# Kernel tuning notes

Measured on AMD Instinct MI355X. Metric: run time of the kernel, lower is better.

The kernel has to match this reference:

```python
import jax, jax.numpy as jnp
import numpy as np

N = 50000        # nodes
E = 800000       # edges (before self-loops)
F_IN = 128       # input features
HID = 32         # per-head hidden channels
H1 = 4           # heads of conv1
H2 = 8           # heads of conv2
NEG_SLOPE = 0.2  # PyG GATConv LeakyReLU slope
E_DEC = 100000   # pos/neg decode edges each


def setup_inputs() -> dict:
    key = jax.random.key(0)
    ks = jax.random.split(key, 12)
    s = 0.1
    return {
        "x": jax.random.normal(ks[0], (N, F_IN), jnp.float32),
        "edge_index": jax.random.randint(ks[1], (2, E), 0, N, dtype=jnp.int32),
        "pos_edge_index": jax.random.randint(ks[2], (2, E_DEC), 0, N, dtype=jnp.int32),
        "neg_edge_index": jax.random.randint(ks[3], (2, E_DEC), 0, N, dtype=jnp.int32),
        "W1": jax.random.normal(ks[4], (F_IN, H1 * HID), jnp.float32) * s,
        "a_src1": jax.random.normal(ks[5], (H1, HID), jnp.float32) * s,
        "a_dst1": jax.random.normal(ks[6], (H1, HID), jnp.float32) * s,
        "b1": jax.random.normal(ks[7], (H1 * HID,), jnp.float32) * s,
        "W2": jax.random.normal(ks[8], (H1 * HID, H2 * HID), jnp.float32) * s,
        "a_src2": jax.random.normal(ks[9], (H2, HID), jnp.float32) * s,
        "a_dst2": jax.random.normal(ks[10], (H2, HID), jnp.float32) * s,
        "b2": jax.random.normal(ks[11], (H2 * HID,), jnp.float32) * s,
    }


def _segment_softmax(e, seg, n):
    # softmax over edges grouped by destination node; max is detached (cancels analytically)
    m = jax.lax.stop_gradient(jax.ops.segment_max(e, seg, num_segments=n))
    ex = jnp.exp(e - m[seg])
    denom = jax.ops.segment_sum(ex, seg, num_segments=n)
    return ex / (denom[seg] + 1e-16)


def _gat_conv(x, src, dst, W, a_src, a_dst, b, heads, out_ch):
    n = x.shape[0]
    h = (x @ W).reshape(n, heads, out_ch)             # [N,H,C]
    al_s = (h * a_src[None]).sum(-1)                  # [N,H]
    al_d = (h * a_dst[None]).sum(-1)                  # [N,H]
    e = al_s[src] + al_d[dst]                         # [E,H] edge logits
    e = jnp.where(e > 0, e, NEG_SLOPE * e)            # LeakyReLU
    alpha = _segment_softmax(e, dst, n)               # [E,H]
    msg = h[src] * alpha[:, :, None]                  # [E,H,C]
    out = jax.ops.segment_sum(msg, dst, num_segments=n)  # [N,H,C]
    return out.reshape(n, heads * out_ch) + b


def reference(x, edge_index, pos_edge_index, neg_edge_index,
              W1, a_src1, a_dst1, b1, W2, a_src2, a_dst2, b2):
    n = x.shape[0]
    loops = jnp.arange(n, dtype=edge_index.dtype)     # PyG add_self_loops=True
    src = jnp.concatenate([edge_index[0], loops])
    dst = jnp.concatenate([edge_index[1], loops])
    # encode
    z = jax.nn.relu(_gat_conv(x, src, dst, W1, a_src1, a_dst1, b1, H1, HID))
    z = _gat_conv(z, src, dst, W2, a_src2, a_dst2, b2, H2, HID)
    # decode
    ei = jnp.concatenate([pos_edge_index, neg_edge_index], axis=1)
    logits = (z[ei[0]] * z[ei[1]]).sum(-1)            # [2*E_DEC]
    return logits
```

## Files before the change

kernel.cpp:

```cpp
#include <hip/hip_runtime.h>
#include <hip/hip_bf16.h>

#define NN 50000
#define EE 800000
#define ET (EE + NN)
#define F_IN 128
#define HID 32
#define H1 4
#define H2 8
#define E_DEC 100000
#define NEG_SLOPE 0.2f

typedef __attribute__((ext_vector_type(8))) short short8;
typedef __attribute__((ext_vector_type(4))) float floatx4;

__device__ __forceinline__ unsigned short f2b(float f) {
    __hip_bfloat16 h = __float2bfloat16(f);
    return *reinterpret_cast<unsigned short*>(&h);
}
__device__ __forceinline__ float b2f(unsigned short u) {
    return __uint_as_float(((unsigned int)u) << 16);
}

__device__ __forceinline__ void packW_one(const float* __restrict__ W,
                                          unsigned short* __restrict__ Wp, int OUT, int id) {
    const int ctg = id >> 8;
    const int ln = id & 63;
    const int col = ctg * 16 + (ln & 15);
    const int k0 = ((id >> 6) & 3) * 32 + ((ln >> 4) & 3) * 8;
    ushort4 lo, hi;
    lo.x = f2b(W[(k0 + 0) * OUT + col]);
    lo.y = f2b(W[(k0 + 1) * OUT + col]);
    lo.z = f2b(W[(k0 + 2) * OUT + col]);
    lo.w = f2b(W[(k0 + 3) * OUT + col]);
    hi.x = f2b(W[(k0 + 4) * OUT + col]);
    hi.y = f2b(W[(k0 + 5) * OUT + col]);
    hi.z = f2b(W[(k0 + 6) * OUT + col]);
    hi.w = f2b(W[(k0 + 7) * OUT + col]);
    ((ushort4*)Wp)[id * 2] = lo;
    ((ushort4*)Wp)[id * 2 + 1] = hi;
}

#define HIST_BLOCKS ((EE / 4 + 255) / 256)
#define PACK_BLOCKS ((6144 + 255) / 256)

__global__ void hist_pack_k(const int* __restrict__ ei, int* __restrict__ counts_p,
                            const int* __restrict__ probe, int* __restrict__ rank,
                            const float* __restrict__ W1, unsigned short* __restrict__ wp1,
                            const float* __restrict__ W2, unsigned short* __restrict__ wp2) {
    if (blockIdx.x < HIST_BLOCKS) {
        const int t = blockIdx.x * 256 + threadIdx.x;
        if (t >= EE / 4) return;
        const int pv = probe[0];
        int* cp = counts_p + (blockIdx.x & 7) * NN;
        const int4 d4 = ((const int4*)(ei + EE))[t];
        int4 r4;
        r4.x = atomicAdd(&cp[d4.x], 1) - pv;
        r4.y = atomicAdd(&cp[d4.y], 1) - pv;
        r4.z = atomicAdd(&cp[d4.z], 1) - pv;
        r4.w = atomicAdd(&cp[d4.w], 1) - pv;
        ((int4*)rank)[t] = r4;
    } else {
        const int id = (blockIdx.x - HIST_BLOCKS) * 256 + threadIdx.x;
        if (id < 2048) packW_one(W1, wp1, 128, id);
        else if (id < 6144) packW_one(W2, wp2, 256, id - 2048);
    }
}

__global__ void scan1_k(const int* __restrict__ counts_p, const int* __restrict__ probe,
                        int* __restrict__ bsum) {
    __shared__ int sh[256];
    const unsigned pv = (unsigned)probe[0];
    int t = threadIdx.x;
    int i = blockIdx.x * 256 + t;
    int deg = 0;
    if (i < NN) {
        unsigned sum = 0;
#pragma unroll
        for (int s = 0; s < 8; ++s) sum += (unsigned)counts_p[s * NN + i];
        deg = (int)(sum - 8u * pv) + 1;
    }
    sh[t] = deg;
    __syncthreads();
    for (int off = 128; off > 0; off >>= 1) {
        if (t < off) sh[t] += sh[t + off];
        __syncthreads();
    }
    if (t == 0) bsum[blockIdx.x] = sh[0];
}

__global__ void scan2_k(int* __restrict__ bsum, int nb, int* __restrict__ start) {
    __shared__ int sh[256];
    int t = threadIdx.x;
    int v = (t < nb) ? bsum[t] : 0;
    sh[t] = v;
    __syncthreads();
    for (int off = 1; off < 256; off <<= 1) {
        int u = (t >= off) ? sh[t - off] : 0;
        __syncthreads();
        sh[t] += u;
        __syncthreads();
    }
    if (t < nb) bsum[t] = sh[t] - v;
    if (t == 0) start[NN] = ET;
}

__global__ void scan3_k(const int* __restrict__ counts_p, const int* __restrict__ probe,
                        const int* __restrict__ bsum, int* __restrict__ start,
                        int* __restrict__ offs, int* __restrict__ csr) {
    __shared__ int sh[256];
    const unsigned pv = (unsigned)probe[0];
    int t = threadIdx.x;
    int i = blockIdx.x * 256 + t;
    int part[8];
    int deg = 0;
    if (i < NN) {
        deg = 1;
#pragma unroll
        for (int s = 0; s < 8; ++s) {
            part[s] = (int)((unsigned)counts_p[s * NN + i] - pv);
            deg += part[s];
        }
    }
    sh[t] = deg;
    __syncthreads();
    for (int off = 1; off < 256; off <<= 1) {
        int u = (t >= off) ? sh[t - off] : 0;
        __syncthreads();
        sh[t] += u;
        __syncthreads();
    }
    int excl = sh[t] - deg + bsum[blockIdx.x];
    if (i < NN) {
        start[i] = excl;
        int o = excl;
#pragma unroll
        for (int s = 0; s < 8; ++s) {
            offs[s * NN + i] = o;
            o += part[s];
        }
        csr[o] = i;
    }
}

__global__ void scatter_k(const int* __restrict__ ei, const int* __restrict__ rank,
                          const int* __restrict__ offs, int* __restrict__ csr) {
    const int t = blockIdx.x * 256 + threadIdx.x;
    if (t >= EE / 4) return;
    const int* off = offs + (blockIdx.x & 7) * NN;
    const int4 s4 = ((const int4*)ei)[t];
    const int4 d4 = ((const int4*)(ei + EE))[t];
    const int4 r4 = ((const int4*)rank)[t];
    csr[off[d4.x] + r4.x] = s4.x;
    csr[off[d4.y] + r4.y] = s4.y;
    csr[off[d4.z] + r4.z] = s4.z;
    csr[off[d4.w] + r4.w] = s4.w;
}

template <int OUT, int H, int CT, bool F32IN>
__global__ void gemm_k(const void* __restrict__ Xin, const unsigned short* __restrict__ Wp,
                       const float* __restrict__ a_src, const float* __restrict__ a_dst,
                       unsigned short* __restrict__ Hout, float* __restrict__ als,
                       float* __restrict__ ald) {
    const int wave = threadIdx.x >> 6;
    const int lane = threadIdx.x & 63;
    const int quad = lane >> 4;
    const int rl = lane & 15;
    const int r0 = blockIdx.x * 64;
    floatx4 acc[4][CT];
#pragma unroll
    for (int rt = 0; rt < 4; ++rt)
#pragma unroll
        for (int ct = 0; ct < CT; ++ct) acc[rt][ct] = {0.f, 0.f, 0.f, 0.f};

#pragma unroll
    for (int ks = 0; ks < 4; ++ks) {
        short8 a[4];
        const int c0k = ks * 32 + quad * 8;
#pragma unroll
        for (int rt = 0; rt < 4; ++rt) {
            int row = r0 + rt * 16 + rl;
            row = row < NN ? row : NN - 1;
            if (F32IN) {
                const float4* xp =
                    (const float4*)((const float*)Xin + (long long)row * 128 + c0k);
                const float4 v0 = xp[0];
                const float4 v1 = xp[1];
                short8 tt;
                tt[0] = (short)f2b(v0.x);
                tt[1] = (short)f2b(v0.y);
                tt[2] = (short)f2b(v0.z);
                tt[3] = (short)f2b(v0.w);
                tt[4] = (short)f2b(v1.x);
                tt[5] = (short)f2b(v1.y);
                tt[6] = (short)f2b(v1.z);
                tt[7] = (short)f2b(v1.w);
                a[rt] = tt;
            } else {
                a[rt] = *(const short8*)((const unsigned short*)Xin +
                                         (long long)row * 128 + c0k);
            }
        }
#pragma unroll
        for (int ct = 0; ct < CT; ++ct) {
            const int ctg = wave * CT + ct;
            const short8 b = *(const short8*)(Wp + (((ctg * 4 + ks) * 64 + lane) << 3));
#pragma unroll
            for (int rt = 0; rt < 4; ++rt)
                acc[rt][ct] = __builtin_amdgcn_mfma_f32_16x16x32_bf16(a[rt], b, acc[rt][ct], 0, 0, 0);
        }
    }
#pragma unroll
    for (int rt = 0; rt < 4; ++rt) {
        const int rowbase = r0 + rt * 16 + quad * 4;
#pragma unroll
        for (int ct = 0; ct < CT; ++ct) {
            const int col = (wave * CT + ct) * 16 + rl;
#pragma unroll
            for (int r = 0; r < 4; ++r) {
                const int row = rowbase + r;
                if (row < NN) Hout[(long long)row * OUT + col] = f2b(acc[rt][ct][r]);
            }
        }
    }
    float asv[CT], adv[CT];
#pragma unroll
    for (int ct = 0; ct < CT; ++ct) {
        const int col = (wave * CT + ct) * 16 + rl;
        asv[ct] = a_src[col];
        adv[ct] = a_dst[col];
    }
#pragma unroll
    for (int rt = 0; rt < 4; ++rt) {
#pragma unroll
        for (int r = 0; r < 4; ++r) {
            const int row = r0 + rt * 16 + quad * 4 + r;
            float ps[CT / 2], pd[CT / 2];
#pragma unroll
            for (int hh = 0; hh < CT / 2; ++hh) {
                ps[hh] = acc[rt][2 * hh][r] * asv[2 * hh] + acc[rt][2 * hh + 1][r] * asv[2 * hh + 1];
                pd[hh] = acc[rt][2 * hh][r] * adv[2 * hh] + acc[rt][2 * hh + 1][r] * adv[2 * hh + 1];
#pragma unroll
                for (int m = 8; m >= 1; m >>= 1) {
                    ps[hh] += __shfl_xor(ps[hh], m, 64);
                    pd[hh] += __shfl_xor(pd[hh], m, 64);
                }
            }
            if (rl == 0 && row < NN) {
#pragma unroll
                for (int hh = 0; hh < CT / 2; ++hh) {
                    const int hd = wave * (CT / 2) + hh;
                    als[(long long)row * H + hd] = ps[hh];
                    ald[(long long)row * H + hd] = pd[hh];
                }
            }
        }
    }
}

__global__ void gather1_k(const int* __restrict__ start, const int* __restrict__ csr,
                          const float* __restrict__ als, const float* __restrict__ ald,
                          const unsigned short* __restrict__ Hin,
                          const float* __restrict__ bias, unsigned short* __restrict__ outp) {
    const int d = blockIdx.x;
    const int lane = threadIdx.x;
    const int cl = lane & 31;
    const int slot = lane >> 5;
    const int hd = cl >> 3;
    const int beg = start[d], end = start[d + 1];
    const float aldd = ald[(long long)d * H1 + hd];
    float a0 = 0.f, a1 = 0.f, a2 = 0.f, a3 = 0.f, den = 0.f;
    int i = beg + slot;
    for (; i + 7 * 2 < end; i += 8 * 2) {
        int s[8];
        float l[8];
        ushort4 hv[8];
#pragma unroll
        for (int k = 0; k < 8; ++k) s[k] = csr[i + k * 2];
#pragma unroll
        for (int k = 0; k < 8; ++k) l[k] = als[(long long)s[k] * H1 + hd] + aldd;
#pragma unroll
        for (int k = 0; k < 8; ++k) hv[k] = *(const ushort4*)(Hin + (long long)s[k] * 128 + cl * 4);
#pragma unroll
        for (int k = 0; k < 8; ++k) {
            float lg = l[k] > 0.f ? l[k] : NEG_SLOPE * l[k];
            const float w = __expf(lg);
            den += w;
            a0 += w * b2f(hv[k].x);
            a1 += w * b2f(hv[k].y);
            a2 += w * b2f(hv[k].z);
            a3 += w * b2f(hv[k].w);
        }
    }
    for (; i + 3 * 2 < end; i += 4 * 2) {
        int s[4];
        float l[4];
        ushort4 hv[4];
#pragma unroll
        for (int k = 0; k < 4; ++k) s[k] = csr[i + k * 2];
#pragma unroll
        for (int k = 0; k < 4; ++k) l[k] = als[(long long)s[k] * H1 + hd] + aldd;
#pragma unroll
        for (int k = 0; k < 4; ++k) hv[k] = *(const ushort4*)(Hin + (long long)s[k] * 128 + cl * 4);
#pragma unroll
        for (int k = 0; k < 4; ++k) {
            float lg = l[k] > 0.f ? l[k] : NEG_SLOPE * l[k];
            const float w = __expf(lg);
            den += w;
            a0 += w * b2f(hv[k].x);
            a1 += w * b2f(hv[k].y);
            a2 += w * b2f(hv[k].z);
            a3 += w * b2f(hv[k].w);
        }
    }
    for (; i < end; i += 2) {
        const int s = csr[i];
        float lg = als[(long long)s * H1 + hd] + aldd;
        lg = lg > 0.f ? lg : NEG_SLOPE * lg;
        const float w = __expf(lg);
        const ushort4 hv = *(const ushort4*)(Hin + (long long)s * 128 + cl * 4);
        den += w;
        a0 += w * b2f(hv.x);
        a1 += w * b2f(hv.y);
        a2 += w * b2f(hv.z);
        a3 += w * b2f(hv.w);
    }
    a0 += __shfl_xor(a0, 32, 64);
    a1 += __shfl_xor(a1, 32, 64);
    a2 += __shfl_xor(a2, 32, 64);
    a3 += __shfl_xor(a3, 32, 64);
    den += __shfl_xor(den, 32, 64);
    if (lane < 32) {
        const float inv = 1.f / (den + 1e-16f);
        const int c0 = cl * 4;
        float v0 = a0 * inv + bias[c0];
        float v1 = a1 * inv + bias[c0 + 1];
        float v2 = a2 * inv + bias[c0 + 2];
        float v3 = a3 * inv + bias[c0 + 3];
        v0 = v0 > 0.f ? v0 : 0.f;
        v1 = v1 > 0.f ? v1 : 0.f;
        v2 = v2 > 0.f ? v2 : 0.f;
        v3 = v3 > 0.f ? v3 : 0.f;
        ushort4 o;
        o.x = f2b(v0);
        o.y = f2b(v1);
        o.z = f2b(v2);
        o.w = f2b(v3);
        *(ushort4*)(outp + (long long)d * 128 + c0) = o;
    }
}

__global__ void gather2_k(const int* __restrict__ start, const int* __restrict__ csr,
                          const float* __restrict__ als, const float* __restrict__ ald,
                          const unsigned short* __restrict__ Hin,
                          const float* __restrict__ bias, unsigned short* __restrict__ outp) {
    const int d = blockIdx.x;
    const int lane = threadIdx.x;
    const int hd = lane >> 3;
    const int beg = start[d], end = start[d + 1];
    const float aldd = ald[(long long)d * H2 + hd];
    float a0 = 0.f, a1 = 0.f, a2 = 0.f, a3 = 0.f, den = 0.f;
    int i = beg;
    for (; i + 7 < end; i += 8) {
        int s[8];
        float l[8];
        ushort4 hv[8];
#pragma unroll
        for (int k = 0; k < 8; ++k) s[k] = csr[i + k];
#pragma unroll
        for (int k = 0; k < 8; ++k) l[k] = als[(long long)s[k] * H2 + hd] + aldd;
#pragma unroll
        for (int k = 0; k < 8; ++k) hv[k] = *(const ushort4*)(Hin + (long long)s[k] * 256 + lane * 4);
#pragma unroll
        for (int k = 0; k < 8; ++k) {
            float lg = l[k] > 0.f ? l[k] : NEG_SLOPE * l[k];
            const float w = __expf(lg);
            den += w;
            a0 += w * b2f(hv[k].x);
            a1 += w * b2f(hv[k].y);
            a2 += w * b2f(hv[k].z);
            a3 += w * b2f(hv[k].w);
        }
    }
    for (; i + 3 < end; i += 4) {
        int s[4];
        float l[4];
        ushort4 hv[4];
#pragma unroll
        for (int k = 0; k < 4; ++k) s[k] = csr[i + k];
#pragma unroll
        for (int k = 0; k < 4; ++k) l[k] = als[(long long)s[k] * H2 + hd] + aldd;
#pragma unroll
        for (int k = 0; k < 4; ++k) hv[k] = *(const ushort4*)(Hin + (long long)s[k] * 256 + lane * 4);
#pragma unroll
        for (int k = 0; k < 4; ++k) {
            float lg = l[k] > 0.f ? l[k] : NEG_SLOPE * l[k];
            const float w = __expf(lg);
            den += w;
            a0 += w * b2f(hv[k].x);
            a1 += w * b2f(hv[k].y);
            a2 += w * b2f(hv[k].z);
            a3 += w * b2f(hv[k].w);
        }
    }
    for (; i < end; ++i) {
        const int s = csr[i];
        float lg = als[(long long)s * H2 + hd] + aldd;
        lg = lg > 0.f ? lg : NEG_SLOPE * lg;
        const float w = __expf(lg);
        const ushort4 hv = *(const ushort4*)(Hin + (long long)s * 256 + lane * 4);
        den += w;
        a0 += w * b2f(hv.x);
        a1 += w * b2f(hv.y);
        a2 += w * b2f(hv.z);
        a3 += w * b2f(hv.w);
    }
    const float inv = 1.f / (den + 1e-16f);
    const int c0 = lane * 4;
    ushort4 o;
    o.x = f2b(a0 * inv + bias[c0]);
    o.y = f2b(a1 * inv + bias[c0 + 1]);
    o.z = f2b(a2 * inv + bias[c0 + 2]);
    o.w = f2b(a3 * inv + bias[c0 + 3]);
    *(ushort4*)(outp + (long long)d * 256 + c0) = o;
}

__global__ void decode_s_k(const int* __restrict__ pei, const int* __restrict__ nei,
                           const unsigned short* __restrict__ z2, float* __restrict__ part) {
    const int s = blockIdx.x & 7;
    const int g = blockIdx.x >> 3;
    const int wave = threadIdx.x >> 6, lane = threadIdx.x & 63;
    const int slot = lane >> 3, cl = lane & 7;
    const int idx = g * 32 + wave * 8 + slot;
    if (idx >= 2 * E_DEC) return;
    int a, b;
    if (idx < E_DEC) {
        a = pei[idx];
        b = pei[E_DEC + idx];
    } else {
        const int j = idx - E_DEC;
        a = nei[j];
        b = nei[E_DEC + j];
    }
    const ushort4 ua = *(const ushort4*)(z2 + (long long)a * 256 + s * 32 + cl * 4);
    const ushort4 ub = *(const ushort4*)(z2 + (long long)b * 256 + s * 32 + cl * 4);
    float sum = b2f(ua.x) * b2f(ub.x) + b2f(ua.y) * b2f(ub.y) +
                b2f(ua.z) * b2f(ub.z) + b2f(ua.w) * b2f(ub.w);
    sum += __shfl_xor(sum, 4, 64);
    sum += __shfl_xor(sum, 2, 64);
    sum += __shfl_xor(sum, 1, 64);
    if (cl == 0) part[(long long)s * (2 * E_DEC) + idx] = sum;
}

__global__ void reduce_k(const float* __restrict__ part, float* __restrict__ out) {
    const int i = blockIdx.x * 256 + threadIdx.x;
    if (i >= 2 * E_DEC) return;
    float s = 0.f;
#pragma unroll
    for (int k = 0; k < 8; ++k) s += part[(long long)k * (2 * E_DEC) + i];
    out[i] = s;
}

extern "C" void kernel_launch(void* const* d_in, const int* in_sizes, int n_in,
                              void* d_out, int out_size, void* d_ws, size_t ws_size,
                              hipStream_t stream) {
    const float* x = (const float*)d_in[0];
    const int* ei = (const int*)d_in[1];
    const int* pei = (const int*)d_in[2];
    const int* nei = (const int*)d_in[3];
    const float* W1 = (const float*)d_in[4];
    const float* as1 = (const float*)d_in[5];
    const float* ad1 = (const float*)d_in[6];
    const float* b1 = (const float*)d_in[7];
    const float* W2 = (const float*)d_in[8];
    const float* as2 = (const float*)d_in[9];
    const float* ad2 = (const float*)d_in[10];
    const float* b2 = (const float*)d_in[11];
    float* out = (float*)d_out;

    unsigned short* h1 = (unsigned short*)d_ws;
    unsigned short* h2 = h1 + (long long)NN * 128;
    unsigned short* z2 = h2 + (long long)NN * 256;
    unsigned short* z1 = z2 + (long long)NN * 256;
    unsigned short* wp1 = z1 + (long long)NN * 128;
    unsigned short* wp2 = wp1 + 128 * 128;
    float* als1 = (float*)(wp2 + 128 * 256);
    float* ald1 = als1 + NN * H1;
    float* als2 = ald1 + NN * H1;
    float* ald2 = als2 + NN * H2;
    float* part = ald2 + NN * H2;
    int* counts_p = (int*)(part + 8 * 2 * E_DEC);
    int* start = counts_p + 8 * NN;
    int* offs = start + NN + 1;
    int* rank = offs + 8 * NN;
    int* bsum = rank + EE;
    int* csr = bsum + 256;
    int* probe = csr + ET;

    const int NB = (NN + 255) / 256;

    hist_pack_k<<<HIST_BLOCKS + PACK_BLOCKS, 256, 0, stream>>>(
        ei, counts_p, probe, rank, W1, wp1, W2, wp2);
    scan1_k<<<NB, 256, 0, stream>>>(counts_p, probe, bsum);
    scan2_k<<<1, 256, 0, stream>>>(bsum, NB, start);
    scan3_k<<<NB, 256, 0, stream>>>(counts_p, probe, bsum, start, offs, csr);
    scatter_k<<<HIST_BLOCKS, 256, 0, stream>>>(ei, rank, offs, csr);

    gemm_k<128, H1, 2, true><<<(NN + 63) / 64, 256, 0, stream>>>(
        x, wp1, as1, ad1, h1, als1, ald1);
    gather1_k<<<NN, 64, 0, stream>>>(start, csr, als1, ald1, h1, b1, z1);

    gemm_k<256, H2, 4, false><<<(NN + 63) / 64, 256, 0, stream>>>(
        z1, wp2, as2, ad2, h2, als2, ald2);
    gather2_k<<<NN, 64, 0, stream>>>(start, csr, als2, ald2, h2, b2, z2);

    decode_s_k<<<8 * ((2 * E_DEC + 31) / 32), 256, 0, stream>>>(pei, nei, z2, part);
    reduce_k<<<(2 * E_DEC + 255) / 256, 256, 0, stream>>>(part, out);
}
```

Before: 334.5 us.

## Store per-head slabs and map head slices to XCDs in gather kernels

The GEMM now writes the projected features as head-major slabs (one [N,32] slab per head) and the attention logits as [H,N]. A single templated gather kernel replaces the two per-layer gathers. Each wave handles one destination node and one head, and the low bits of the block index pick the head slice, so each XCD's L2 only touches one head's slab. The goal is better L2 locality for random source gathers, at the cost of more blocks, re-reading the CSR once per head, and dropping the unrolled multi-load loops, which lowers memory-level parallelism per lane.

```diff
diff --git a/kernel.cpp b/kernel.cpp
--- a/kernel.cpp
+++ b/kernel.cpp
@@ -216,10 +216,11 @@
 #pragma unroll
         for (int ct = 0; ct < CT; ++ct) {
             const int col = (wave * CT + ct) * 16 + rl;
+            unsigned short* hp = Hout + (long long)(col >> 5) * NN * 32 + (col & 31);
 #pragma unroll
             for (int r = 0; r < 4; ++r) {
                 const int row = rowbase + r;
-                if (row < NN) Hout[(long long)row * OUT + col] = f2b(acc[rt][ct][r]);
+                if (row < NN) hp[(long long)row * 32] = f2b(acc[rt][ct][r]);
             }
         }
     }
@@ -250,179 +251,75 @@
 #pragma unroll
                 for (int hh = 0; hh < CT / 2; ++hh) {
                     const int hd = wave * (CT / 2) + hh;
-                    als[(long long)row * H + hd] = ps[hh];
-                    ald[(long long)row * H + hd] = pd[hh];
+                    als[(long long)hd * NN + row] = ps[hh];
+                    ald[(long long)hd * NN + row] = pd[hh];
                 }
             }
         }
     }
 }
 
-__global__ void gather1_k(const int* __restrict__ start, const int* __restrict__ csr,
+template <int OUT, int NSLICE, bool RELU>
+__global__ void gathers_k(const int* __restrict__ start, const int* __restrict__ csr,
                           const float* __restrict__ als, const float* __restrict__ ald,
                           const unsigned short* __restrict__ Hin,
                           const float* __restrict__ bias, unsigned short* __restrict__ outp) {
-    const int d = blockIdx.x;
-    const int lane = threadIdx.x;
-    const int cl = lane & 31;
-    const int slot = lane >> 5;
-    const int hd = cl >> 3;
+    constexpr int SUB = 8 / NSLICE;
+    const int xcd = blockIdx.x & 7;
+    const int s = xcd / SUB;
+    const int sub = xcd & (SUB - 1);
+    const int wave = threadIdx.x >> 6;
+    const int lane = threadIdx.x & 63;
+    const int cl = lane & 7;
+    const int slot = lane >> 3;
+    const int d = (blockIdx.x >> 3) * (4 * SUB) + sub * 4 + wave;
+    if (d >= NN) return;
+    const float* als_h = als + (long long)s * NN;
+    const float aldd = ald[(long long)s * NN + d];
+    const unsigned short* slab = Hin + (long long)s * NN * 32;
     const int beg = start[d], end = start[d + 1];
-    const float aldd = ald[(long long)d * H1 + hd];
     float a0 = 0.f, a1 = 0.f, a2 = 0.f, a3 = 0.f, den = 0.f;
-    int i = beg + slot;
-    for (; i + 7 * 2 < end; i += 8 * 2) {
-        int s[8];
-        float l[8];
-        ushort4 hv[8];
-#pragma unroll
-        for (int k = 0; k < 8; ++k) s[k] = csr[i + k * 2];
-#pragma unroll
-        for (int k = 0; k < 8; ++k) l[k] = als[(long long)s[k] * H1 + hd] + aldd;
-#pragma unroll
-        for (int k = 0; k < 8; ++k) hv[k] = *(const ushort4*)(Hin + (long long)s[k] * 128 + cl * 4);
-#pragma unroll
-        for (int k = 0; k < 8; ++k) {
-            float lg = l[k] > 0.f ? l[k] : NEG_SLOPE * l[k];
-            const float w = __expf(lg);
-            den += w;
-            a0 += w * b2f(hv[k].x);
-            a1 += w * b2f(hv[k].y);
-            a2 += w * b2f(hv[k].z);
-            a3 += w * b2f(hv[k].w);
-        }
-    }
-    for (; i + 3 * 2 < end; i += 4 * 2) {
-        int s[4];
-        float l[4];
-        ushort4 hv[4];
-#pragma unroll
-        for (int k = 0; k < 4; ++k) s[k] = csr[i + k * 2];
-#pragma unroll
-        for (int k = 0; k < 4; ++k) l[k] = als[(long long)s[k] * H1 + hd] + aldd;
-#pragma unroll
-        for (int k = 0; k < 4; ++k) hv[k] = *(const ushort4*)(Hin + (long long)s[k] * 128 + cl * 4);
-#pragma unroll
-        for (int k = 0; k < 4; ++k) {
-            float lg = l[k] > 0.f ? l[k] : NEG_SLOPE * l[k];
-            const float w = __expf(lg);
-            den += w;
-            a0 += w * b2f(hv[k].x);
-            a1 += w * b2f(hv[k].y);
-            a2 += w * b2f(hv[k].z);
-            a3 += w * b2f(hv[k].w);
-        }
-    }
-    for (; i < end; i += 2) {
-        const int s = csr[i];
-        float lg = als[(long long)s * H1 + hd] + aldd;
+    for (int i = beg + slot; i < end; i += 8) {
+        const int src = __builtin_nontemporal_load(csr + i);
+        float lg = als_h[src] + aldd;
         lg = lg > 0.f ? lg : NEG_SLOPE * lg;
         const float w = __expf(lg);
-        const ushort4 hv = *(const ushort4*)(Hin + (long long)s * 128 + cl * 4);
+        const ushort4 hv = *(const ushort4*)(slab + (long long)src * 32 + cl * 4);
         den += w;
         a0 += w * b2f(hv.x);
         a1 += w * b2f(hv.y);
         a2 += w * b2f(hv.z);
         a3 += w * b2f(hv.w);
     }
-    a0 += __shfl_xor(a0, 32, 64);
-    a1 += __shfl_xor(a1, 32, 64);
-    a2 += __shfl_xor(a2, 32, 64);
-    a3 += __shfl_xor(a3, 32, 64);
-    den += __shfl_xor(den, 32, 64);
-    if (lane < 32) {
+#pragma unroll
+    for (int m = 8; m < 64; m <<= 1) {
+        a0 += __shfl_xor(a0, m, 64);
+        a1 += __shfl_xor(a1, m, 64);
+        a2 += __shfl_xor(a2, m, 64);
+        a3 += __shfl_xor(a3, m, 64);
+        den += __shfl_xor(den, m, 64);
+    }
+    if (lane < 8) {
         const float inv = 1.f / (den + 1e-16f);
-        const int c0 = cl * 4;
+        const int c0 = s * 32 + cl * 4;
         float v0 = a0 * inv + bias[c0];
         float v1 = a1 * inv + bias[c0 + 1];
         float v2 = a2 * inv + bias[c0 + 2];
         float v3 = a3 * inv + bias[c0 + 3];
-        v0 = v0 > 0.f ? v0 : 0.f;
-        v1 = v1 > 0.f ? v1 : 0.f;
-        v2 = v2 > 0.f ? v2 : 0.f;
-        v3 = v3 > 0.f ? v3 : 0.f;
-        ushort4 o;
-        o.x = f2b(v0);
-        o.y = f2b(v1);
-        o.z = f2b(v2);
-        o.w = f2b(v3);
-        *(ushort4*)(outp + (long long)d * 128 + c0) = o;
-    }
-}
-
-__global__ void gather2_k(const int* __restrict__ start, const int* __restrict__ csr,
-                          const float* __restrict__ als, const float* __restrict__ ald,
-                          const unsigned short* __restrict__ Hin,
-                          const float* __restrict__ bias, unsigned short* __restrict__ outp) {
-    const int d = blockIdx.x;
-    const int lane = threadIdx.x;
-    const int hd = lane >> 3;
-    const int beg = start[d], end = start[d + 1];
-    const float aldd = ald[(long long)d * H2 + hd];
-    float a0 = 0.f, a1 = 0.f, a2 = 0.f, a3 = 0.f, den = 0.f;
-    int i = beg;
-    for (; i + 7 < end; i += 8) {
-        int s[8];
-        float l[8];
-        ushort4 hv[8];
-#pragma unroll
-        for (int k = 0; k < 8; ++k) s[k] = csr[i + k];
-#pragma unroll
-        for (int k = 0; k < 8; ++k) l[k] = als[(long long)s[k] * H2 + hd] + aldd;
-#pragma unroll
-        for (int k = 0; k < 8; ++k) hv[k] = *(const ushort4*)(Hin + (long long)s[k] * 256 + lane * 4);
-#pragma unroll
-        for (int k = 0; k < 8; ++k) {
-            float lg = l[k] > 0.f ? l[k] : NEG_SLOPE * l[k];
-            const float w = __expf(lg);
-            den += w;
-            a0 += w * b2f(hv[k].x);
-            a1 += w * b2f(hv[k].y);
-            a2 += w * b2f(hv[k].z);
-            a3 += w * b2f(hv[k].w);
-        }
-    }
-    for (; i + 3 < end; i += 4) {
-        int s[4];
-        float l[4];
-        ushort4 hv[4];
-#pragma unroll
-        for (int k = 0; k < 4; ++k) s[k] = csr[i + k];
-#pragma unroll
-        for (int k = 0; k < 4; ++k) l[k] = als[(long long)s[k] * H2 + hd] + aldd;
-#pragma unroll
-        for (int k = 0; k < 4; ++k) hv[k] = *(const ushort4*)(Hin + (long long)s[k] * 256 + lane * 4);
-#pragma unroll
-        for (int k = 0; k < 4; ++k) {
-            float lg = l[k] > 0.f ? l[k] : NEG_SLOPE * l[k];
-            const float w = __expf(lg);
-            den += w;
-            a0 += w * b2f(hv[k].x);
-            a1 += w * b2f(hv[k].y);
-            a2 += w * b2f(hv[k].z);
-            a3 += w * b2f(hv[k].w);
-        }
-    }
-    for (; i < end; ++i) {
-        const int s = csr[i];
-        float lg = als[(long long)s * H2 + hd] + aldd;
-        lg = lg > 0.f ? lg : NEG_SLOPE * lg;
-        const float w = __expf(lg);
-        const ushort4 hv = *(const ushort4*)(Hin + (long long)s * 256 + lane * 4);
-        den += w;
-        a0 += w * b2f(hv.x);
-        a1 += w * b2f(hv.y);
-        a2 += w * b2f(hv.z);
-        a3 += w * b2f(hv.w);
-    }
-    const float inv = 1.f / (den + 1e-16f);
-    const int c0 = lane * 4;
-    ushort4 o;
-    o.x = f2b(a0 * inv + bias[c0]);
-    o.y = f2b(a1 * inv + bias[c0 + 1]);
-    o.z = f2b(a2 * inv + bias[c0 + 2]);
-    o.w = f2b(a3 * inv + bias[c0 + 3]);
-    *(ushort4*)(outp + (long long)d * 256 + c0) = o;
+        if (RELU) {
+            v0 = v0 > 0.f ? v0 : 0.f;
+            v1 = v1 > 0.f ? v1 : 0.f;
+            v2 = v2 > 0.f ? v2 : 0.f;
+            v3 = v3 > 0.f ? v3 : 0.f;
+        }
+        unsigned long long pk =
+            (unsigned long long)f2b(v0) |
+            ((unsigned long long)f2b(v1) << 16) |
+            ((unsigned long long)f2b(v2) << 32) |
+            ((unsigned long long)f2b(v3) << 48);
+        __builtin_nontemporal_store(
+            pk, (unsigned long long*)(outp + (long long)d * OUT + c0));
+    }
 }
 
 __global__ void decode_s_k(const int* __restrict__ pei, const int* __restrict__ nei,
@@ -508,11 +405,13 @@
 
     gemm_k<128, H1, 2, true><<<(NN + 63) / 64, 256, 0, stream>>>(
         x, wp1, as1, ad1, h1, als1, ald1);
-    gather1_k<<<NN, 64, 0, stream>>>(start, csr, als1, ald1, h1, b1, z1);
+    gathers_k<128, 4, true><<<8 * ((NN + 7) / 8), 256, 0, stream>>>(
+        start, csr, als1, ald1, h1, b1, z1);
 
     gemm_k<256, H2, 4, false><<<(NN + 63) / 64, 256, 0, stream>>>(
         z1, wp2, as2, ad2, h2, als2, ald2);
-    gather2_k<<<NN, 64, 0, stream>>>(start, csr, als2, ald2, h2, b2, z2);
+    gathers_k<256, 8, false><<<8 * ((NN + 3) / 4), 256, 0, stream>>>(
+        start, csr, als2, ald2, h2, b2, z2);
 
     decode_s_k<<<8 * ((2 * E_DEC + 31) / 32), 256, 0, stream>>>(pei, nei, z2, part);
     reduce_k<<<(2 * E_DEC + 255) / 256, 256, 0, stream>>>(part, out);
```

Measured after the change: 498.0 us. +48.9%, slower.
